# Kernel optimization log

Measured on AMD Instinct MI355X. Metric: run time of the kernel, lower is better.

The kernel has to match this reference:

```python
import jax, jax.numpy as jnp
import numpy as np
from jax import lax

# Config (matches init_kwargs)
B, CIN, H, W = 32, 256, 56, 56
COUT, KS, STRIDE, PAD, GROUPS = 256, 3, 1, 1, 2
CG_IN = CIN // GROUPS            # 128
OUT_F = COUT // GROUPS           # 128 per-group out features
IN_F = CG_IN * KS * KS           # 1152 per-group in features
Q = (IN_F * OUT_F // 4) * GROUPS # 73728 quadruplets total
TAU = 1.0

# All six 2-of-4 masking patterns (as in the torch module)
_MASK_PATTERNS = np.array([[0.,0.,1.,1.],[0.,1.,0.,1.],[0.,1.,1.,0.],
                           [1.,0.,0.,1.],[1.,0.,1.,0.],[1.,1.,0.,0.]], dtype=np.float32)


def setup_inputs() -> dict:
    key = jax.random.key(0)
    k1, k2, k3, k4 = jax.random.split(key, 4)
    x = jax.random.normal(k1, (B, CIN, H, W), dtype=jnp.float32)
    # per-group weight blocks, xavier-ish scale
    Ws = jax.random.normal(k2, (GROUPS, OUT_F, IN_F), dtype=jnp.float32) * 0.03
    choice_weights = jax.random.normal(k3, (Q, 6), dtype=jnp.float32)
    # gumbel noise: -log(Exp(1)) ~ Gumbel(0,1), matching -empty.exponential_().log()
    gumbels = -jnp.log(jax.random.exponential(k4, (Q, 6), dtype=jnp.float32))
    masking_patterns = jnp.asarray(_MASK_PATTERNS)
    return {"x": x, "Ws": Ws, "choice_weights": choice_weights,
            "gumbels": gumbels, "masking_patterns": masking_patterns}


def _hard_gumbel_softmax(logits, gumbels, tau):
    # straight-through hard gumbel softmax over last dim
    y_soft = jax.nn.softmax((logits + gumbels) / tau, axis=-1)
    idx = jnp.argmax(y_soft, axis=-1)
    y_hard = jax.nn.one_hot(idx, logits.shape[-1], dtype=logits.dtype)
    return y_hard - lax.stop_gradient(y_soft) + y_soft


def reference(x, Ws, choice_weights, gumbels, masking_patterns):
    # 1) sample 2:4 mask per quadruplet via hard gumbel-softmax choice over 6 patterns
    choice = _hard_gumbel_softmax(choice_weights, gumbels, TAU)   # (Q, 6)
    mask = choice @ masking_patterns                              # (Q, 4)
    mask = mask.reshape(GROUPS, OUT_F, IN_F)                      # quadruplets tile W row-major
    Wm = Ws * mask                                                # (G, OUT_F, IN_F)

    # 2) im2col (torch Unfold ordering: channel-major, then kh, kw)
    patches = lax.conv_general_dilated_patches(
        x, filter_shape=(KS, KS), window_strides=(STRIDE, STRIDE),
        padding=[(PAD, PAD), (PAD, PAD)])                         # (B, CIN*KS*KS, Ho, Wo)
    Ho = (H + 2 * PAD - KS) // STRIDE + 1
    Wo = (W + 2 * PAD - KS) // STRIDE + 1
    L = Ho * Wo
    # channel-major ordering => group g occupies contiguous IN_F rows
    patches = patches.reshape(B, GROUPS, IN_F, L)                 # (B, G, IN_F, L)

    # 3) per-group masked GEMM, no bias (use_bias=False)
    y = jnp.einsum('goi,bgil->bgol', Wm, patches)                 # (B, G, OUT_F, L)
    return y.reshape(B, COUT, Ho, Wo)
```

## Files before the change

### kernel.cpp

```cpp
#include <hip/hip_runtime.h>


#define INF   1152
#define HO    56
#define LOUT  3136
#define XP    58

typedef __attribute__((ext_vector_type(8))) short bf16x8;
typedef __attribute__((ext_vector_type(4))) float f32x4;

__device__ __forceinline__ unsigned short f2bf(float f) {
  union { float f; unsigned u; } v; v.f = f;
  unsigned r = v.u + 0x7fffu + ((v.u >> 16) & 1u);
  return (unsigned short)(r >> 16);
}

__device__ __forceinline__ void async_load16(const void* g, void* l) {
  __builtin_amdgcn_global_load_lds(
      (const __attribute__((address_space(1))) void*)g,
      (__attribute__((address_space(3))) void*)l, 16, 0, 0);
}

__global__ __launch_bounds__(256) void mask_pack_kernel(
    const float* __restrict__ Ws, const float* __restrict__ cw,
    const float* __restrict__ gb, const float* __restrict__ pat,
    unsigned short* __restrict__ Wt) {
  int idx = blockIdx.x * 256 + threadIdx.x;
  int c   = idx & 127;
  int of  = (idx >> 7) & 127;
  int gt  = idx >> 14;
  int g   = gt / 9;
  int tap = gt - g * 9;
  int e   = ((g << 7) + of) * INF + c * 9 + tap;
  int q   = e >> 2;
  int pos = e & 3;
  const float* cq = cw + q * 6;
  const float* gq = gb + q * 6;
  float best = cq[0] + gq[0]; int bi = 0;
  #pragma unroll
  for (int j = 1; j < 6; ++j) {
    float v = cq[j] + gq[j];
    if (v > best) { best = v; bi = j; }
  }
  float m = pat[bi * 4 + pos];
  Wt[idx] = f2bf(Ws[e] * m);
}

__global__ __launch_bounds__(256) void xpose_kernel(const float* __restrict__ x,
                                                    unsigned short* __restrict__ Xt) {
  __shared__ float lds[56 * 129];
  const int t   = threadIdx.x;
  const int ihp = blockIdx.x;
  const int bg  = blockIdx.y;
  unsigned int* dst = (unsigned int*)(Xt + ((bg * XP + ihp) * XP) * 128);
  if (ihp == 0 || ihp == XP - 1) {
    for (int i = t; i < XP * 64; i += 256) dst[i] = 0u;
    return;
  }
  const int ih = ihp - 1;
  const float* src = x + (bg * 128) * LOUT + ih * HO;
  for (int i = t; i < 128 * HO; i += 256) {
    int c = i / HO, iw = i - c * HO;
    lds[iw * 129 + c] = src[c * LOUT + iw];
  }
  __syncthreads();
  for (int i = t; i < XP * 64; i += 256) {
    int iwp = i >> 6;
    int cp  = i & 63;
    unsigned int val = 0;
    if (iwp != 0 && iwp != XP - 1) {
      int iw = iwp - 1, c = cp << 1;
      unsigned lo = f2bf(lds[iw * 129 + c]);
      unsigned hi = f2bf(lds[iw * 129 + c + 1]);
      val = lo | (hi << 16);
    }
    dst[i] = val;
  }
}

__global__ __launch_bounds__(256, 2) void conv_mfma_kernel(
    const unsigned short* __restrict__ Wt, const unsigned short* __restrict__ Xt,
    float* __restrict__ out) {
  __shared__ __align__(16) unsigned short sA[128 * 32];
  __shared__ __align__(16) unsigned short sB[128 * 32];
  const int t  = threadIdx.x;
  const int ln = t & 63, wv = t >> 6;
  const int wm = wv >> 1, wn = wv & 1;
  const int col = ln & 15, kq = ln >> 4;
  const int tileN = blockIdx.x;
  const int bg    = blockIdx.y;
  const int g     = bg & 1;
  const int l0    = tileN << 7;

  const int c8   = (t & 3) << 3;
  const int aoff = ((t >> 2) << 7) + c8;
  int boff[2];
  #pragma unroll
  for (int p = 0; p < 2; ++p) {
    int ll = l0 + (p << 6) + (t >> 2);
    if (ll > LOUT - 1) ll = LOUT - 1;
    int oh = ll / HO, ow = ll - oh * HO;
    boff[p] = ((bg * XP + oh) * XP + ow) * 128 + c8;
  }
  const int ldsw = (wv << 9);

  f32x4 acc[4][4];
  #pragma unroll
  for (int i = 0; i < 4; ++i)
    #pragma unroll
    for (int j = 0; j < 4; ++j) acc[i][j] = (f32x4){0.f, 0.f, 0.f, 0.f};

  for (int tap = 0; tap < 9; ++tap) {
    const int th = tap / 3, tw = tap - th * 3;
    const int bTap = (th * XP + tw) << 7;
    const int aTap = (g * 9 + tap) << 14;
    #pragma unroll 1
    for (int kc = 0; kc < 4; ++kc) {
      const int c0 = kc << 5;
      __syncthreads();
      #pragma unroll
      for (int p = 0; p < 2; ++p) {
        async_load16(Wt + aTap + (p << 13) + aoff + c0, &sA[(p << 11) + ldsw]);
        async_load16(Xt + boff[p] + bTap + c0,          &sB[(p << 11) + ldsw]);
      }
      __syncthreads();
      bf16x8 af[4], bfr[4];
      #pragma unroll
      for (int mi = 0; mi < 4; ++mi)
        af[mi] = *(const bf16x8*)&sA[(((wm << 6) + (mi << 4) + col) << 5) + (kq << 3)];
      #pragma unroll
      for (int ni = 0; ni < 4; ++ni)
        bfr[ni] = *(const bf16x8*)&sB[(((wn << 6) + (ni << 4) + col) << 5) + (kq << 3)];
      #pragma unroll
      for (int mi = 0; mi < 4; ++mi)
        #pragma unroll
        for (int ni = 0; ni < 4; ++ni)
          acc[mi][ni] = __builtin_amdgcn_mfma_f32_16x16x32_bf16(
              af[mi], bfr[ni], acc[mi][ni], 0, 0, 0);
    }
  }

  const int rowq = kq << 2;
  #pragma unroll
  for (int mi = 0; mi < 4; ++mi) {
    #pragma unroll
    for (int ni = 0; ni < 4; ++ni) {
      const int l = l0 + (wn << 6) + (ni << 4) + col;
      if (l < LOUT) {
        #pragma unroll
        for (int r = 0; r < 4; ++r) {
          const int of = (wm << 6) + (mi << 4) + rowq + r;
          out[(bg * 128 + of) * LOUT + l] = acc[mi][ni][r];
        }
      }
    }
  }
}

extern "C" void kernel_launch(void* const* d_in, const int* in_sizes, int n_in,
                              void* d_out, int out_size, void* d_ws, size_t ws_size,
                              hipStream_t stream) {
  const float* x   = (const float*)d_in[0];
  const float* Ws  = (const float*)d_in[1];
  const float* cw  = (const float*)d_in[2];
  const float* gb  = (const float*)d_in[3];
  const float* pat = (const float*)d_in[4];
  float* out = (float*)d_out;

  unsigned short* Wt = (unsigned short*)d_ws;
  unsigned short* Xt = (unsigned short*)((char*)d_ws + (1 << 20));

  mask_pack_kernel<<<1152, 256, 0, stream>>>(Ws, cw, gb, pat, Wt);
  xpose_kernel<<<dim3(XP, 64), 256, 0, stream>>>(x, Xt);
  conv_mfma_kernel<<<dim3(25, 64), 256, 0, stream>>>(Wt, Xt, out);
}
```

Measured before the change: 278.0 us.

## Split mask sampling, vectorize transpose, swizzle LDS, remap blocks, raise occupancy

Splits mask generation into a per-quadruplet argmax kernel and a separate pack kernel, so the 6-way argmax runs once per quadruplet instead of once per weight element. The input transpose now uses float4 loads and 16-byte bf16 stores. The conv kernel gets an XOR swizzle on the LDS k-chunk to reduce bank conflicts, a block-index remap that interleaves tiles, and a launch-bounds occupancy hint raised from 2 to 4. These are several unrelated changes, and the higher occupancy hint may force register spilling given the 64-float accumulators.

```diff
diff --git a/kernel.cpp b/kernel.cpp
--- a/kernel.cpp
+++ b/kernel.cpp
@@ -5,6 +5,7 @@
 #define HO    56
 #define LOUT  3136
 #define XP    58
+#define Q     73728
 
 typedef __attribute__((ext_vector_type(8))) short bf16x8;
 typedef __attribute__((ext_vector_type(4))) float f32x4;
@@ -21,19 +22,10 @@
       (__attribute__((address_space(3))) void*)l, 16, 0, 0);
 }
 
-__global__ __launch_bounds__(256) void mask_pack_kernel(
-    const float* __restrict__ Ws, const float* __restrict__ cw,
-    const float* __restrict__ gb, const float* __restrict__ pat,
-    unsigned short* __restrict__ Wt) {
-  int idx = blockIdx.x * 256 + threadIdx.x;
-  int c   = idx & 127;
-  int of  = (idx >> 7) & 127;
-  int gt  = idx >> 14;
-  int g   = gt / 9;
-  int tap = gt - g * 9;
-  int e   = ((g << 7) + of) * INF + c * 9 + tap;
-  int q   = e >> 2;
-  int pos = e & 3;
+__global__ __launch_bounds__(256) void gumbel_kernel(
+    const float* __restrict__ cw, const float* __restrict__ gb,
+    unsigned char* __restrict__ pmask) {
+  int q = blockIdx.x * 256 + threadIdx.x;
   const float* cq = cw + q * 6;
   const float* gq = gb + q * 6;
   float best = cq[0] + gq[0]; int bi = 0;
@@ -42,7 +34,20 @@
     float v = cq[j] + gq[j];
     if (v > best) { best = v; bi = j; }
   }
-  float m = pat[bi * 4 + pos];
+  pmask[q] = (unsigned char)bi;
+}
+
+__global__ __launch_bounds__(256) void pack_kernel(
+    const float* __restrict__ Ws, const unsigned char* __restrict__ pmask,
+    const float* __restrict__ pat, unsigned short* __restrict__ Wt) {
+  int idx = blockIdx.x * 256 + threadIdx.x;
+  int c   = idx & 127;
+  int of  = (idx >> 7) & 127;
+  int gt  = idx >> 14;
+  int g   = gt / 9;
+  int tap = gt - g * 9;
+  int e   = ((g << 7) + of) * INF + c * 9 + tap;
+  float m = pat[pmask[e >> 2] * 4 + (e & 3)];
   Wt[idx] = f2bf(Ws[e] * m);
 }
 
@@ -52,33 +57,40 @@
   const int t   = threadIdx.x;
   const int ihp = blockIdx.x;
   const int bg  = blockIdx.y;
-  unsigned int* dst = (unsigned int*)(Xt + ((bg * XP + ihp) * XP) * 128);
+  uint4* dst = (uint4*)(Xt + ((bg * XP + ihp) * XP) * 128);
   if (ihp == 0 || ihp == XP - 1) {
-    for (int i = t; i < XP * 64; i += 256) dst[i] = 0u;
+    const uint4 z = {0u, 0u, 0u, 0u};
+    for (int i = t; i < XP * 16; i += 256) dst[i] = z;
     return;
   }
   const int ih = ihp - 1;
-  const float* src = x + (bg * 128) * LOUT + ih * HO;
-  for (int i = t; i < 128 * HO; i += 256) {
-    int c = i / HO, iw = i - c * HO;
-    lds[iw * 129 + c] = src[c * LOUT + iw];
+  const float4* src = (const float4*)(x + (bg * 128) * LOUT + ih * HO);
+  for (int i = t; i < 128 * 14; i += 256) {
+    int c = i / 14, seg = i - c * 14;
+    float4 v = src[c * (LOUT / 4) + seg];
+    float* row = &lds[(seg * 4) * 129 + c];
+    row[0]       = v.x;
+    row[129]     = v.y;
+    row[2 * 129] = v.z;
+    row[3 * 129] = v.w;
   }
   __syncthreads();
-  for (int i = t; i < XP * 64; i += 256) {
-    int iwp = i >> 6;
-    int cp  = i & 63;
-    unsigned int val = 0;
+  for (int i = t; i < XP * 16; i += 256) {
+    int iwp = i >> 4, oct = i & 15;
+    uint4 val = {0u, 0u, 0u, 0u};
     if (iwp != 0 && iwp != XP - 1) {
-      int iw = iwp - 1, c = cp << 1;
-      unsigned lo = f2bf(lds[iw * 129 + c]);
-      unsigned hi = f2bf(lds[iw * 129 + c + 1]);
-      val = lo | (hi << 16);
+      const float* s = &lds[(iwp - 1) * 129 + (oct << 3)];
+      unsigned d0 = (unsigned)f2bf(s[0]) | ((unsigned)f2bf(s[1]) << 16);
+      unsigned d1 = (unsigned)f2bf(s[2]) | ((unsigned)f2bf(s[3]) << 16);
+      unsigned d2 = (unsigned)f2bf(s[4]) | ((unsigned)f2bf(s[5]) << 16);
+      unsigned d3 = (unsigned)f2bf(s[6]) | ((unsigned)f2bf(s[7]) << 16);
+      val.x = d0; val.y = d1; val.z = d2; val.w = d3;
     }
     dst[i] = val;
   }
 }
 
-__global__ __launch_bounds__(256, 2) void conv_mfma_kernel(
+__global__ __launch_bounds__(256, 4) void conv_mfma_kernel(
     const unsigned short* __restrict__ Wt, const unsigned short* __restrict__ Xt,
     float* __restrict__ out) {
   __shared__ __align__(16) unsigned short sA[128 * 32];
@@ -87,12 +99,16 @@
   const int ln = t & 63, wv = t >> 6;
   const int wm = wv >> 1, wn = wv & 1;
   const int col = ln & 15, kq = ln >> 4;
-  const int tileN = blockIdx.x;
-  const int bg    = blockIdx.y;
+
+  const int lid   = blockIdx.y * 25 + blockIdx.x;
+  const int v     = (lid & 7) * 200 + (lid >> 3);
+  const int bg    = v / 25;
+  const int tileN = v - bg * 25;
   const int g     = bg & 1;
   const int l0    = tileN << 7;
 
-  const int c8   = (t & 3) << 3;
+  const int kqs  = (t & 3) ^ ((t >> 3) & 3);
+  const int c8   = kqs << 3;
   const int aoff = ((t >> 2) << 7) + c8;
   int boff[2];
   #pragma unroll
@@ -103,6 +119,7 @@
     boff[p] = ((bg * XP + oh) * XP + ow) * 128 + c8;
   }
   const int ldsw = (wv << 9);
+  const int swk  = (kq ^ ((col >> 1) & 3)) << 3;
 
   f32x4 acc[4][4];
   #pragma unroll
@@ -127,10 +144,10 @@
       bf16x8 af[4], bfr[4];
       #pragma unroll
       for (int mi = 0; mi < 4; ++mi)
-        af[mi] = *(const bf16x8*)&sA[(((wm << 6) + (mi << 4) + col) << 5) + (kq << 3)];
+        af[mi] = *(const bf16x8*)&sA[(wm << 11) + (((mi << 4) + col) << 5) + swk];
       #pragma unroll
       for (int ni = 0; ni < 4; ++ni)
-        bfr[ni] = *(const bf16x8*)&sB[(((wn << 6) + (ni << 4) + col) << 5) + (kq << 3)];
+        bfr[ni] = *(const bf16x8*)&sB[(wn << 11) + (((ni << 4) + col) << 5) + swk];
       #pragma unroll
       for (int mi = 0; mi < 4; ++mi)
         #pragma unroll
@@ -167,10 +184,12 @@
   const float* pat = (const float*)d_in[4];
   float* out = (float*)d_out;
 
-  unsigned short* Wt = (unsigned short*)d_ws;
-  unsigned short* Xt = (unsigned short*)((char*)d_ws + (1 << 20));
+  unsigned short* Wt    = (unsigned short*)d_ws;
+  unsigned char*  pmask = (unsigned char*)((char*)d_ws + 640 * 1024);
+  unsigned short* Xt    = (unsigned short*)((char*)d_ws + (1 << 20));
 
-  mask_pack_kernel<<<1152, 256, 0, stream>>>(Ws, cw, gb, pat, Wt);
+  gumbel_kernel<<<Q / 256, 256, 0, stream>>>(cw, gb, pmask);
   xpose_kernel<<<dim3(XP, 64), 256, 0, stream>>>(x, Xt);
+  pack_kernel<<<1152, 256, 0, stream>>>(Ws, pmask, pat, Wt);
   conv_mfma_kernel<<<dim3(25, 64), 256, 0, stream>>>(Wt, Xt, out);
 }
```

Result: no change. 278.0 us (-0.0%).
